# Performance work log

Hardware: AMD Instinct MI355X
Metric: run time of the kernel (lower is better)

The kernel has to match this reference:

```python
import jax, jax.numpy as jnp
import numpy as np

B, S, D, H = 2048, 200, 128, 4
H1, H2 = 64, 32
F = 4 * D
TIME_DECAY = 0.1


def setup_inputs() -> dict:
    key = jax.random.key(0)
    ks = jax.random.split(key, 10)
    query = jax.random.normal(ks[0], (B, D), dtype=jnp.float32)
    keys = jax.random.normal(ks[1], (B, S, D), dtype=jnp.float32)
    keys_mask = jax.random.randint(ks[2], (B, S), 0, 2).astype(bool)
    keys_mask = keys_mask.at[:, 0].set(True)  # avoid fully-masked rows
    sc = 0.02
    # per-head MLP params, stacked over heads
    W1 = sc * jax.random.normal(ks[3], (H, H1, F), dtype=jnp.float32)
    b1 = jnp.zeros((H, H1), dtype=jnp.float32)
    a1 = 0.25 * jnp.ones((H,), dtype=jnp.float32)  # PReLU (default single param)
    W2 = sc * jax.random.normal(ks[4], (H, H2, H1), dtype=jnp.float32)
    b2 = jnp.zeros((H, H2), dtype=jnp.float32)
    a2 = 0.25 * jnp.ones((H,), dtype=jnp.float32)
    W3 = sc * jax.random.normal(ks[5], (H, H2), dtype=jnp.float32)
    b3 = jnp.zeros((H,), dtype=jnp.float32)
    Wo = sc * jax.random.normal(ks[6], (D, D), dtype=jnp.float32)
    bo = jnp.zeros((D,), dtype=jnp.float32)
    return {"query": query, "keys": keys, "keys_mask": keys_mask,
            "W1": W1, "b1": b1, "a1": a1, "W2": W2, "b2": b2, "a2": a2,
            "W3": W3, "b3": b3, "Wo": Wo, "bo": bo}


def reference(query, keys, keys_mask, W1, b1, a1, W2, b2, a2, W3, b3, Wo, bo):
    b, s, d = keys.shape
    q = query[:, None, :]                                    # [B,1,D]
    x = jnp.concatenate(
        [keys, jnp.broadcast_to(q, (b, s, d)), keys * q, keys - q], axis=-1)  # [B,S,4D]
    pos = jnp.arange(s, dtype=keys.dtype)
    tw = jnp.exp(TIME_DECAY * (pos - s + 1))                 # [S]
    # all heads batched: [B,H,S,H1]
    h = jnp.einsum('bsf,hdf->bhsd', x, W1) + b1[None, :, None, :]
    h = jnp.where(h >= 0, h, a1[None, :, None, None] * h)    # PReLU
    h = jnp.einsum('bhsd,hed->bhse', h, W2) + b2[None, :, None, :]
    h = jnp.where(h >= 0, h, a2[None, :, None, None] * h)
    scores = jnp.einsum('bhse,he->bhs', h, W3) + b3[None, :, None]
    scores = scores * tw[None, None, :]
    scores = jnp.where(keys_mask[:, None, :], scores, -1e9)
    w = jax.nn.softmax(scores, axis=-1)                      # [B,H,S]
    out_h = jnp.einsum('bhs,bsd->bhd', w, keys)              # [B,H,D]
    combined = out_h.mean(axis=1)                            # [B,D]
    output = combined @ Wo.T + bo                            # [B,D]
    avg_weights = w.mean(axis=1)                             # [B,S]
    return output, avg_weights
```

## Files before the change

### kernel.cpp

```cpp
#include <hip/hip_runtime.h>
#include <hip/hip_bf16.h>
#include <stdint.h>

#define Bsz 2048
#define Ssz 200
#define Dsz 128
#define SP  224

typedef __attribute__((ext_vector_type(8))) short short8;
typedef __attribute__((ext_vector_type(4))) float f32x4;
typedef unsigned short ushort_t;
typedef unsigned int uint_t;

#define KEYS_OFF   0
#define H1S_OFF    51200
#define SCW_OFF    67584
#define C1S_OFF    71168
#define SMEM_BYTES 72192
#define SCWB_OFF   51200
#define COMB_OFF   59392
#define PO2_OFF    59904

__device__ __forceinline__ ushort_t cvtbf(float x) {
    __hip_bfloat16 h = __float2bfloat16(x);
    ushort_t u;
    __builtin_memcpy(&u, &h, 2);
    return u;
}

__global__ void prep_kernel(const float* __restrict__ W1, const float* __restrict__ W2,
                            const float* __restrict__ Wo,
                            float* __restrict__ W1sum, float* __restrict__ W1c,
                            float* __restrict__ W1diffR, float* __restrict__ WoT,
                            ushort_t* __restrict__ W2bf) {
    int i = blockIdx.x * blockDim.x + threadIdx.x;
    if (i < 32768) {
        int n = i >> 7, j = i & 127;
        float a  = W1[n * 512 + j];
        float dd = W1[n * 512 + 384 + j];
        W1sum[i] = a + dd;
        W1c[i]   = W1[n * 512 + 256 + j];
        W1diffR[i] = W1[n * 512 + 128 + j] - dd;
    }
    if (i < 16384) {
        int j = i >> 7, d = i & 127;
        WoT[i] = Wo[d * 128 + j];
    }
    if (i < 8192) W2bf[i] = cvtbf(W2[i]);
}

__launch_bounds__(256, 2)
__global__ void attn_kernel(const float* __restrict__ query, const float* __restrict__ keys,
                            const int* __restrict__ kmask,
                            const float* __restrict__ a1, const float* __restrict__ b2,
                            const float* __restrict__ a2, const float* __restrict__ W3,
                            const float* __restrict__ b3, const float* __restrict__ b1,
                            const float* __restrict__ bo,
                            const float* __restrict__ W1sum, const float* __restrict__ W1c,
                            const float* __restrict__ W1diffR,
                            const float* __restrict__ WoT, const ushort_t* __restrict__ W2bf,
                            float* __restrict__ out) {
    extern __shared__ char smem[];
    const int tid = threadIdx.x;
    const int bb  = blockIdx.x;
    const int w   = tid >> 6;
    const int l   = tid & 63;
    const int l15 = l & 15;
    const int lk  = l >> 4;

    float* scw  = (float*)(smem + SCW_OFF);
    float* c1s  = (float*)(smem + C1S_OFF);
    float* comb = (float*)(smem + COMB_OFF);
    float* po2  = (float*)(smem + PO2_OFF);
    const float* kb = keys + (size_t)bb * Ssz * Dsz;

    #pragma unroll
    for (int it = 0; it < 25; ++it) {
        int id = tid + 256 * it;
        int row = id >> 5, c4 = id & 31;
        float4 kv = *(const float4*)(kb + (size_t)row * Dsz + c4 * 4);
        uint2 p;
        p.x = (uint_t)cvtbf(kv.x) | ((uint_t)cvtbf(kv.y) << 16);
        p.y = (uint_t)cvtbf(kv.z) | ((uint_t)cvtbf(kv.w) << 16);
        int off = KEYS_OFF + (((row << 8) + (c4 << 3)) ^ ((row & 7) << 4));
        *(uint2*)(smem + off) = p;
    }

    {
        float accc = b1[tid];
        const float4* wr  = (const float4*)(W1diffR + tid * 128);
        const float4* qv4 = (const float4*)(query + bb * 128);
        #pragma unroll 8
        for (int j4 = 0; j4 < 32; ++j4) {
            float4 wv = wr[j4];
            float4 qq = qv4[j4];
            accc += wv.x * qq.x + wv.y * qq.y + wv.z * qq.z + wv.w * qq.w;
        }
        c1s[tid] = accc;
    }

    short8 bfr[16];
    #pragma unroll
    for (int t = 0; t < 4; ++t) {
        const int k0 = t * 32 + lk * 8;
        const float4* pq = (const float4*)(query + bb * 128 + k0);
        float4 q0 = pq[0], q1 = pq[1];
        #pragma unroll
        for (int nt = 0; nt < 4; ++nt) {
            int n = w * 64 + nt * 16 + l15;
            const float4* ps = (const float4*)(W1sum + n * 128 + k0);
            const float4* pc = (const float4*)(W1c + n * 128 + k0);
            float4 s0 = ps[0], s1 = ps[1];
            float4 c0 = pc[0], c1f = pc[1];
            short8 ov;
            ov[0] = (short)cvtbf(s0.x + c0.x * q0.x);
            ov[1] = (short)cvtbf(s0.y + c0.y * q0.y);
            ov[2] = (short)cvtbf(s0.z + c0.z * q0.z);
            ov[3] = (short)cvtbf(s0.w + c0.w * q0.w);
            ov[4] = (short)cvtbf(s1.x + c1f.x * q1.x);
            ov[5] = (short)cvtbf(s1.y + c1f.y * q1.y);
            ov[6] = (short)cvtbf(s1.z + c1f.z * q1.z);
            ov[7] = (short)cvtbf(s1.w + c1f.w * q1.w);
            bfr[t * 4 + nt] = ov;
        }
    }

    const float a1v = a1[w];
    const float a2v = a2[w];
    const float b3v = b3[w];
    float b2v[2], w3v[2];
    #pragma unroll
    for (int nt = 0; nt < 2; ++nt) {
        b2v[nt] = b2[w * 32 + nt * 16 + l15];
        w3v[nt] = W3[w * 32 + nt * 16 + l15];
    }
    short8 w2f[2][2];
    #pragma unroll
    for (int kt = 0; kt < 2; ++kt)
        #pragma unroll
        for (int nt = 0; nt < 2; ++nt)
            w2f[kt][nt] = *(const short8*)(W2bf + w * 2048 + (nt * 16 + l15) * 64 + kt * 32 + lk * 8);

    __syncthreads();

    float c1v[4];
    #pragma unroll
    for (int nt = 0; nt < 4; ++nt) c1v[nt] = c1s[w * 64 + nt * 16 + l15];

    const f32x4 fz = {0.f, 0.f, 0.f, 0.f};
    char* h1base = smem + H1S_OFF + w * 4096;

    #pragma unroll 2
    for (int m = 0; m < 13; ++m) {
        char* h1b = h1base + (m & 1) * 2048;
        f32x4 acc[4];
        #pragma unroll
        for (int nt = 0; nt < 4; ++nt) acc[nt] = fz;

        #pragma unroll
        for (int t = 0; t < 4; ++t) {
            int row = m * 16 + l15;
            row = (row < Ssz) ? row : (Ssz - 1);
            int off = KEYS_OFF + (((row << 8) + (t * 64 + lk * 16)) ^ ((row & 7) << 4));
            short8 afr = *(const short8*)(smem + off);
            #pragma unroll
            for (int nt = 0; nt < 4; ++nt)
                acc[nt] = __builtin_amdgcn_mfma_f32_16x16x32_bf16(afr, bfr[t * 4 + nt], acc[nt], 0, 0, 0);
        }

        #pragma unroll
        for (int nt = 0; nt < 4; ++nt) {
            #pragma unroll
            for (int r = 0; r < 4; ++r) {
                float v = acc[nt][r] + c1v[nt];
                v = (v >= 0.f) ? v : a1v * v;
                int lr = lk * 4 + r;
                int colb = (nt * 16 + l15) * 2;
                *(ushort_t*)(h1b + lr * 128 + (colb ^ ((lr & 7) << 4))) = cvtbf(v);
            }
        }

        f32x4 acc2[2];
        acc2[0] = fz; acc2[1] = fz;
        #pragma unroll
        for (int kt = 0; kt < 2; ++kt) {
            short8 afr2 = *(const short8*)(h1b + l15 * 128 + ((kt * 64 + lk * 16) ^ ((l15 & 7) << 4)));
            #pragma unroll
            for (int nt = 0; nt < 2; ++nt)
                acc2[nt] = __builtin_amdgcn_mfma_f32_16x16x32_bf16(afr2, w2f[kt][nt], acc2[nt], 0, 0, 0);
        }
        #pragma unroll
        for (int r = 0; r < 4; ++r) {
            float sum = 0.f;
            #pragma unroll
            for (int nt = 0; nt < 2; ++nt) {
                float v = acc2[nt][r] + b2v[nt];
                v = (v >= 0.f) ? v : a2v * v;
                sum += v * w3v[nt];
            }
            sum += __shfl_xor(sum, 1);
            sum += __shfl_xor(sum, 2);
            sum += __shfl_xor(sum, 4);
            sum += __shfl_xor(sum, 8);
            if (l15 == 0) {
                int sg = m * 16 + lk * 4 + r;
                if (sg < Ssz) {
                    float tw = __expf(0.1f * (float)(sg - (Ssz - 1)));
                    float sc = (sum + b3v) * tw;
                    scw[w * SP + sg] = kmask[bb * Ssz + sg] ? sc : -1.0e9f;
                }
            }
        }
    }

    float wv[4];
    {
        float xv[4];
        float mx = -3.0e38f;
        #pragma unroll
        for (int i = 0; i < 4; ++i) {
            int s = l + 64 * i;
            xv[i] = (s < Ssz) ? scw[w * SP + s] : -1.0e30f;
            mx = fmaxf(mx, xv[i]);
        }
        #pragma unroll
        for (int m = 1; m < 64; m <<= 1) mx = fmaxf(mx, __shfl_xor(mx, m));
        float sm = 0.f;
        #pragma unroll
        for (int i = 0; i < 4; ++i) {
            int s = l + 64 * i;
            wv[i] = (s < Ssz) ? __expf(xv[i] - mx) : 0.f;
            sm += wv[i];
        }
        #pragma unroll
        for (int m = 1; m < 64; m <<= 1) sm += __shfl_xor(sm, m);
        float inv = 1.0f / sm;
        #pragma unroll
        for (int i = 0; i < 4; ++i) {
            int s = l + 64 * i;
            wv[i] *= inv;
            if (s < Ssz) scw[w * SP + s] = wv[i];
        }
    }
    __syncthreads();

    #pragma unroll
    for (int i = 0; i < 4; ++i) {
        int s = l + 64 * i;
        *(ushort_t*)(smem + SCWB_OFF + w * 512 + s * 2) =
            (s < Ssz) ? cvtbf(wv[i]) : (ushort_t)0;
    }
    {
        uint_t* zb = (uint_t*)(smem + SCWB_OFF + 4 * 512);
        #pragma unroll
        for (int k = 0; k < 6; ++k) zb[tid + 256 * k] = 0;
    }
    __syncthreads();

    if (tid < Ssz) {
        float aw = 0.25f * (scw[tid] + scw[SP + tid] + scw[2 * SP + tid] + scw[3 * SP + tid]);
        out[Bsz * Dsz + bb * Ssz + tid] = aw;
    }

    {
        f32x4 acc4a = fz, acc4b = fz;
        #pragma unroll
        for (int t7 = 0; t7 < 7; ++t7) {
            int kbase = t7 * 32 + lk * 8;
            short8 afr = *(const short8*)(smem + SCWB_OFF + l15 * 512 + kbase * 2);
            short8 b2a, b2b;
            #pragma unroll
            for (int j = 0; j < 8; ++j) {
                int s = kbase + j;
                ushort_t kva = 0, kvb = 0;
                if (s < Ssz) {
                    int rowoff = KEYS_OFF + (s << 8);
                    int sw = (s & 7) << 4;
                    kva = *(const ushort_t*)(smem + (rowoff + ((32 * w + l15) << 1) ^ sw));
                    kvb = *(const ushort_t*)(smem + (rowoff + ((32 * w + 16 + l15) << 1) ^ sw));
                }
                b2a[j] = (short)kva;
                b2b[j] = (short)kvb;
            }
            acc4a = __builtin_amdgcn_mfma_f32_16x16x32_bf16(afr, b2a, acc4a, 0, 0, 0);
            acc4b = __builtin_amdgcn_mfma_f32_16x16x32_bf16(afr, b2b, acc4b, 0, 0, 0);
        }
        if (lk == 0) {
            comb[32 * w + l15]      = 0.25f * (acc4a[0] + acc4a[1] + acc4a[2] + acc4a[3]);
            comb[32 * w + 16 + l15] = 0.25f * (acc4b[0] + acc4b[1] + acc4b[2] + acc4b[3]);
        }
    }
    __syncthreads();

    {
        int d = tid & 127, part = tid >> 7;
        float o = 0.f;
        const float* wp = WoT + (size_t)part * 64 * 128 + d;
        #pragma unroll 8
        for (int j = 0; j < 64; ++j) o += comb[part * 64 + j] * wp[j * 128];
        po2[part * 128 + d] = o;
    }
    __syncthreads();
    if (tid < 128) out[bb * Dsz + tid] = bo[tid] + po2[tid] + po2[128 + tid];
}

extern "C" void kernel_launch(void* const* d_in, const int* in_sizes, int n_in,
                              void* d_out, int out_size, void* d_ws, size_t ws_size,
                              hipStream_t stream) {
    const float* query = (const float*)d_in[0];
    const float* keys  = (const float*)d_in[1];
    const int*   kmask = (const int*)d_in[2];
    const float* W1    = (const float*)d_in[3];
    const float* b1    = (const float*)d_in[4];
    const float* a1    = (const float*)d_in[5];
    const float* W2    = (const float*)d_in[6];
    const float* b2    = (const float*)d_in[7];
    const float* a2    = (const float*)d_in[8];
    const float* W3    = (const float*)d_in[9];
    const float* b3    = (const float*)d_in[10];
    const float* Wo    = (const float*)d_in[11];
    const float* bo    = (const float*)d_in[12];
    float* out = (float*)d_out;

    char* ws = (char*)d_ws;
    float*    W1sum   = (float*)(ws);
    float*    W1c     = (float*)(ws + 131072);
    float*    W1diffR = (float*)(ws + 262144);
    float*    WoT     = (float*)(ws + 393216);
    ushort_t* W2bf    = (ushort_t*)(ws + 458752);

    hipFuncSetAttribute(reinterpret_cast<const void*>(attn_kernel),
                        hipFuncAttributeMaxDynamicSharedMemorySize, SMEM_BYTES);

    prep_kernel<<<128, 256, 0, stream>>>(W1, W2, Wo, W1sum, W1c, W1diffR, WoT, W2bf);
    attn_kernel<<<Bsz, 256, SMEM_BYTES, stream>>>(query, keys, kmask, a1, b2, a2, W3, b3, b1, bo,
                                                  W1sum, W1c, W1diffR, WoT, W2bf, out);
}
```

Baseline: 209.7 us.

## Double block size to 512 threads and split sequence tiles across two wave halves

The attention kernel now launches 512 threads per block. Each head gets two waves that split the 13 sequence tiles of the MLP scoring loop between them, and the weighted-sum and output-projection stages are re-partitioned over 8 waves. The h1 staging buffer is no longer double-buffered per wave. The launch bounds are raised to request more waves per execution unit. The aim is more latency hiding and MFMA parallelism per block, at the risk of tighter register budgets (the B-fragments alone take many VGPRs) and extra synchronisation.

```diff
diff --git a/kernel.cpp b/kernel.cpp
--- a/kernel.cpp
+++ b/kernel.cpp
@@ -49,7 +49,7 @@
     if (i < 8192) W2bf[i] = cvtbf(W2[i]);
 }
 
-__launch_bounds__(256, 2)
+__launch_bounds__(512, 4)
 __global__ void attn_kernel(const float* __restrict__ query, const float* __restrict__ keys,
                             const int* __restrict__ kmask,
                             const float* __restrict__ a1, const float* __restrict__ b2,
@@ -63,7 +63,9 @@
     extern __shared__ char smem[];
     const int tid = threadIdx.x;
     const int bb  = blockIdx.x;
-    const int w   = tid >> 6;
+    const int w    = tid >> 6;
+    const int h    = w & 3;
+    const int half = w >> 2;
     const int l   = tid & 63;
     const int l15 = l & 15;
     const int lk  = l >> 4;
@@ -75,26 +77,28 @@
     const float* kb = keys + (size_t)bb * Ssz * Dsz;
 
     #pragma unroll
-    for (int it = 0; it < 25; ++it) {
-        int id = tid + 256 * it;
-        int row = id >> 5, c4 = id & 31;
-        float4 kv = *(const float4*)(kb + (size_t)row * Dsz + c4 * 4);
-        uint2 p;
-        p.x = (uint_t)cvtbf(kv.x) | ((uint_t)cvtbf(kv.y) << 16);
-        p.y = (uint_t)cvtbf(kv.z) | ((uint_t)cvtbf(kv.w) << 16);
-        int off = KEYS_OFF + (((row << 8) + (c4 << 3)) ^ ((row & 7) << 4));
-        *(uint2*)(smem + off) = p;
-    }
-
-    {
+    for (int it = 0; it < 13; ++it) {
+        int id = tid + 512 * it;
+        if (id < 6400) {
+            int row = id >> 5, c4 = id & 31;
+            float4 kv = *(const float4*)(kb + (size_t)row * Dsz + c4 * 4);
+            uint2 p;
+            p.x = (uint_t)cvtbf(kv.x) | ((uint_t)cvtbf(kv.y) << 16);
+            p.y = (uint_t)cvtbf(kv.z) | ((uint_t)cvtbf(kv.w) << 16);
+            int off = KEYS_OFF + (((row << 8) + (c4 << 3)) ^ ((row & 7) << 4));
+            *(uint2*)(smem + off) = p;
+        }
+    }
+
+    if (tid < 256) {
         float accc = b1[tid];
         const float4* wr  = (const float4*)(W1diffR + tid * 128);
         const float4* qv4 = (const float4*)(query + bb * 128);
         #pragma unroll 8
         for (int j4 = 0; j4 < 32; ++j4) {
-            float4 wv = wr[j4];
+            float4 wvv = wr[j4];
             float4 qq = qv4[j4];
-            accc += wv.x * qq.x + wv.y * qq.y + wv.z * qq.z + wv.w * qq.w;
+            accc += wvv.x * qq.x + wvv.y * qq.y + wvv.z * qq.z + wvv.w * qq.w;
         }
         c1s[tid] = accc;
     }
@@ -107,7 +111,7 @@
         float4 q0 = pq[0], q1 = pq[1];
         #pragma unroll
         for (int nt = 0; nt < 4; ++nt) {
-            int n = w * 64 + nt * 16 + l15;
+            int n = h * 64 + nt * 16 + l15;
             const float4* ps = (const float4*)(W1sum + n * 128 + k0);
             const float4* pc = (const float4*)(W1c + n * 128 + k0);
             float4 s0 = ps[0], s1 = ps[1];
@@ -125,97 +129,99 @@
         }
     }
 
-    const float a1v = a1[w];
-    const float a2v = a2[w];
-    const float b3v = b3[w];
+    const float a1v = a1[h];
+    const float a2v = a2[h];
+    const float b3v = b3[h];
     float b2v[2], w3v[2];
     #pragma unroll
     for (int nt = 0; nt < 2; ++nt) {
-        b2v[nt] = b2[w * 32 + nt * 16 + l15];
-        w3v[nt] = W3[w * 32 + nt * 16 + l15];
+        b2v[nt] = b2[h * 32 + nt * 16 + l15];
+        w3v[nt] = W3[h * 32 + nt * 16 + l15];
     }
     short8 w2f[2][2];
     #pragma unroll
     for (int kt = 0; kt < 2; ++kt)
         #pragma unroll
         for (int nt = 0; nt < 2; ++nt)
-            w2f[kt][nt] = *(const short8*)(W2bf + w * 2048 + (nt * 16 + l15) * 64 + kt * 32 + lk * 8);
+            w2f[kt][nt] = *(const short8*)(W2bf + h * 2048 + (nt * 16 + l15) * 64 + kt * 32 + lk * 8);
 
     __syncthreads();
 
     float c1v[4];
     #pragma unroll
-    for (int nt = 0; nt < 4; ++nt) c1v[nt] = c1s[w * 64 + nt * 16 + l15];
+    for (int nt = 0; nt < 4; ++nt) c1v[nt] = c1s[h * 64 + nt * 16 + l15];
 
     const f32x4 fz = {0.f, 0.f, 0.f, 0.f};
-    char* h1base = smem + H1S_OFF + w * 4096;
-
-    #pragma unroll 2
-    for (int m = 0; m < 13; ++m) {
-        char* h1b = h1base + (m & 1) * 2048;
-        f32x4 acc[4];
-        #pragma unroll
-        for (int nt = 0; nt < 4; ++nt) acc[nt] = fz;
-
-        #pragma unroll
-        for (int t = 0; t < 4; ++t) {
-            int row = m * 16 + l15;
-            row = (row < Ssz) ? row : (Ssz - 1);
-            int off = KEYS_OFF + (((row << 8) + (t * 64 + lk * 16)) ^ ((row & 7) << 4));
-            short8 afr = *(const short8*)(smem + off);
-            #pragma unroll
-            for (int nt = 0; nt < 4; ++nt)
-                acc[nt] = __builtin_amdgcn_mfma_f32_16x16x32_bf16(afr, bfr[t * 4 + nt], acc[nt], 0, 0, 0);
-        }
-
-        #pragma unroll
-        for (int nt = 0; nt < 4; ++nt) {
+    char* h1b = smem + H1S_OFF + w * 2048;
+
+    #pragma unroll 1
+    for (int mi = 0; mi < 7; ++mi) {
+        int m = half * 7 + mi;
+        if (m < 13) {
+            f32x4 acc[4];
+            #pragma unroll
+            for (int nt = 0; nt < 4; ++nt) acc[nt] = fz;
+
+            #pragma unroll
+            for (int t = 0; t < 4; ++t) {
+                int row = m * 16 + l15;
+                row = (row < Ssz) ? row : (Ssz - 1);
+                int off = KEYS_OFF + (((row << 8) + (t * 64 + lk * 16)) ^ ((row & 7) << 4));
+                short8 afr = *(const short8*)(smem + off);
+                #pragma unroll
+                for (int nt = 0; nt < 4; ++nt)
+                    acc[nt] = __builtin_amdgcn_mfma_f32_16x16x32_bf16(afr, bfr[t * 4 + nt], acc[nt], 0, 0, 0);
+            }
+
+            #pragma unroll
+            for (int nt = 0; nt < 4; ++nt) {
+                #pragma unroll
+                for (int r = 0; r < 4; ++r) {
+                    float v = acc[nt][r] + c1v[nt];
+                    v = (v >= 0.f) ? v : a1v * v;
+                    int lr = lk * 4 + r;
+                    int colb = (nt * 16 + l15) * 2;
+                    *(ushort_t*)(h1b + lr * 128 + (colb ^ ((lr & 7) << 4))) = cvtbf(v);
+                }
+            }
+
+            f32x4 acc2[2];
+            acc2[0] = fz; acc2[1] = fz;
+            #pragma unroll
+            for (int kt = 0; kt < 2; ++kt) {
+                short8 afr2 = *(const short8*)(h1b + l15 * 128 + ((kt * 64 + lk * 16) ^ ((l15 & 7) << 4)));
+                #pragma unroll
+                for (int nt = 0; nt < 2; ++nt)
+                    acc2[nt] = __builtin_amdgcn_mfma_f32_16x16x32_bf16(afr2, w2f[kt][nt], acc2[nt], 0, 0, 0);
+            }
             #pragma unroll
             for (int r = 0; r < 4; ++r) {
-                float v = acc[nt][r] + c1v[nt];
-                v = (v >= 0.f) ? v : a1v * v;
-                int lr = lk * 4 + r;
-                int colb = (nt * 16 + l15) * 2;
-                *(ushort_t*)(h1b + lr * 128 + (colb ^ ((lr & 7) << 4))) = cvtbf(v);
-            }
-        }
-
-        f32x4 acc2[2];
-        acc2[0] = fz; acc2[1] = fz;
-        #pragma unroll
-        for (int kt = 0; kt < 2; ++kt) {
-            short8 afr2 = *(const short8*)(h1b + l15 * 128 + ((kt * 64 + lk * 16) ^ ((l15 & 7) << 4)));
-            #pragma unroll
-            for (int nt = 0; nt < 2; ++nt)
-                acc2[nt] = __builtin_amdgcn_mfma_f32_16x16x32_bf16(afr2, w2f[kt][nt], acc2[nt], 0, 0, 0);
-        }
-        #pragma unroll
-        for (int r = 0; r < 4; ++r) {
-            float sum = 0.f;
-            #pragma unroll
-            for (int nt = 0; nt < 2; ++nt) {
-                float v = acc2[nt][r] + b2v[nt];
-                v = (v >= 0.f) ? v : a2v * v;
-                sum += v * w3v[nt];
-            }
-            sum += __shfl_xor(sum, 1);
-            sum += __shfl_xor(sum, 2);
-            sum += __shfl_xor(sum, 4);
-            sum += __shfl_xor(sum, 8);
-            if (l15 == 0) {
-                int sg = m * 16 + lk * 4 + r;
-                if (sg < Ssz) {
-                    float tw = __expf(0.1f * (float)(sg - (Ssz - 1)));
-                    float sc = (sum + b3v) * tw;
-                    scw[w * SP + sg] = kmask[bb * Ssz + sg] ? sc : -1.0e9f;
+                float sum = 0.f;
+                #pragma unroll
+                for (int nt = 0; nt < 2; ++nt) {
+                    float v = acc2[nt][r] + b2v[nt];
+                    v = (v >= 0.f) ? v : a2v * v;
+                    sum += v * w3v[nt];
                 }
-            }
-        }
-    }
-
-    float wv[4];
-    {
-        float xv[4];
+                sum += __shfl_xor(sum, 1);
+                sum += __shfl_xor(sum, 2);
+                sum += __shfl_xor(sum, 4);
+                sum += __shfl_xor(sum, 8);
+                if (l15 == 0) {
+                    int sg = m * 16 + lk * 4 + r;
+                    if (sg < Ssz) {
+                        float tw = __expf(0.1f * (float)(sg - (Ssz - 1)));
+                        float sc = (sum + b3v) * tw;
+                        scw[h * SP + sg] = kmask[bb * Ssz + sg] ? sc : -1.0e9f;
+                    }
+                }
+            }
+        }
+    }
+    __syncthreads();
+
+    if (w < 4) {
+        float wv[4], xv[4];
         float mx = -3.0e38f;
         #pragma unroll
         for (int i = 0; i < 4; ++i) {
@@ -240,20 +246,14 @@
             int s = l + 64 * i;
             wv[i] *= inv;
             if (s < Ssz) scw[w * SP + s] = wv[i];
-        }
-    }
-    __syncthreads();
-
-    #pragma unroll
-    for (int i = 0; i < 4; ++i) {
-        int s = l + 64 * i;
-        *(ushort_t*)(smem + SCWB_OFF + w * 512 + s * 2) =
-            (s < Ssz) ? cvtbf(wv[i]) : (ushort_t)0;
-    }
-    {
+            *(ushort_t*)(smem + SCWB_OFF + w * 512 + s * 2) =
+                (s < Ssz) ? cvtbf(wv[i]) : (ushort_t)0;
+        }
+    } else {
         uint_t* zb = (uint_t*)(smem + SCWB_OFF + 4 * 512);
-        #pragma unroll
-        for (int k = 0; k < 6; ++k) zb[tid + 256 * k] = 0;
+        int t4 = tid - 256;
+        #pragma unroll
+        for (int k = 0; k < 6; ++k) zb[t4 + 256 * k] = 0;
     }
     __syncthreads();
 
@@ -263,45 +263,41 @@
     }
 
     {
-        f32x4 acc4a = fz, acc4b = fz;
+        f32x4 acc4 = fz;
         #pragma unroll
         for (int t7 = 0; t7 < 7; ++t7) {
             int kbase = t7 * 32 + lk * 8;
             short8 afr = *(const short8*)(smem + SCWB_OFF + l15 * 512 + kbase * 2);
-            short8 b2a, b2b;
+            short8 bfr2;
             #pragma unroll
             for (int j = 0; j < 8; ++j) {
                 int s = kbase + j;
-                ushort_t kva = 0, kvb = 0;
+                ushort_t kv = 0;
                 if (s < Ssz) {
-                    int rowoff = KEYS_OFF + (s << 8);
-                    int sw = (s & 7) << 4;
-                    kva = *(const ushort_t*)(smem + (rowoff + ((32 * w + l15) << 1) ^ sw));
-                    kvb = *(const ushort_t*)(smem + (rowoff + ((32 * w + 16 + l15) << 1) ^ sw));
+                    kv = *(const ushort_t*)(smem + KEYS_OFF +
+                          ((((s << 8) + ((16 * w + l15) << 1))) ^ ((s & 7) << 4)));
                 }
-                b2a[j] = (short)kva;
-                b2b[j] = (short)kvb;
-            }
-            acc4a = __builtin_amdgcn_mfma_f32_16x16x32_bf16(afr, b2a, acc4a, 0, 0, 0);
-            acc4b = __builtin_amdgcn_mfma_f32_16x16x32_bf16(afr, b2b, acc4b, 0, 0, 0);
-        }
-        if (lk == 0) {
-            comb[32 * w + l15]      = 0.25f * (acc4a[0] + acc4a[1] + acc4a[2] + acc4a[3]);
-            comb[32 * w + 16 + l15] = 0.25f * (acc4b[0] + acc4b[1] + acc4b[2] + acc4b[3]);
-        }
+                bfr2[j] = (short)kv;
+            }
+            acc4 = __builtin_amdgcn_mfma_f32_16x16x32_bf16(afr, bfr2, acc4, 0, 0, 0);
+        }
+        if (lk == 0)
+            comb[16 * w + l15] = 0.25f * (acc4[0] + acc4[1] + acc4[2] + acc4[3]);
     }
     __syncthreads();
 
     {
         int d = tid & 127, part = tid >> 7;
         float o = 0.f;
-        const float* wp = WoT + (size_t)part * 64 * 128 + d;
+        const float* wp = WoT + (size_t)part * 32 * 128 + d;
         #pragma unroll 8
-        for (int j = 0; j < 64; ++j) o += comb[part * 64 + j] * wp[j * 128];
+        for (int j = 0; j < 32; ++j) o += comb[part * 32 + j] * wp[j * 128];
         po2[part * 128 + d] = o;
     }
     __syncthreads();
-    if (tid < 128) out[bb * Dsz + tid] = bo[tid] + po2[tid] + po2[128 + tid];
+    if (tid < 128) {
+        out[bb * Dsz + tid] = bo[tid] + po2[tid] + po2[128 + tid] + po2[256 + tid] + po2[384 + tid];
+    }
 }
 
 extern "C" void kernel_launch(void* const* d_in, const int* in_sizes, int n_in,
@@ -333,6 +329,6 @@
                         hipFuncAttributeMaxDynamicSharedMemorySize, SMEM_BYTES);
 
     prep_kernel<<<128, 256, 0, stream>>>(W1, W2, Wo, W1sum, W1c, W1diffR, WoT, W2bf);
-    attn_kernel<<<Bsz, 256, SMEM_BYTES, stream>>>(query, keys, kmask, a1, b2, a2, W3, b3, b1, bo,
+    attn_kernel<<<Bsz, 512, SMEM_BYTES, stream>>>(query, keys, kmask, a1, b2, a2, W3, b3, b1, bo,
                                                   W1sum, W1c, W1diffR, WoT, W2bf, out);
 }
```

Result: slower. 292.7 us (+39.6%).

## Split fused attention kernel into c1, per-half-sequence scores, and finish kernels

Applied to the files above, without the earlier changes.

Breaks the single per-batch kernel into three launches. A separate kernel precomputes the query-dependent bias, a scores kernel handles half the sequence per block with less shared memory and higher occupancy, and a finish kernel does softmax, weighted key sum and the output projection. The aim is more parallelism and occupancy for the MLP scoring phase. The cost is extra launches, a round trip of scores through global memory, reloading keys in fp32 in the finish kernel, and the bfr weight fragments being rebuilt twice per batch row.

```diff
diff --git a/kernel.cpp b/kernel.cpp
--- a/kernel.cpp
+++ b/kernel.cpp
@@ -5,7 +5,6 @@
 #define Bsz 2048
 #define Ssz 200
 #define Dsz 128
-#define SP  224
 
 typedef __attribute__((ext_vector_type(8))) short short8;
 typedef __attribute__((ext_vector_type(4))) float f32x4;
@@ -13,13 +12,9 @@
 typedef unsigned int uint_t;
 
 #define KEYS_OFF   0
-#define H1S_OFF    51200
-#define SCW_OFF    67584
-#define C1S_OFF    71168
-#define SMEM_BYTES 72192
-#define SCWB_OFF   51200
-#define COMB_OFF   59392
-#define PO2_OFF    59904
+#define H1S_OFF    28672
+#define C1S_OFF    36864
+#define SMEM_A     37888
 
 __device__ __forceinline__ ushort_t cvtbf(float x) {
     __hip_bfloat16 h = __float2bfloat16(x);
@@ -49,36 +44,50 @@
     if (i < 8192) W2bf[i] = cvtbf(W2[i]);
 }
 
-__launch_bounds__(256, 2)
-__global__ void attn_kernel(const float* __restrict__ query, const float* __restrict__ keys,
-                            const int* __restrict__ kmask,
-                            const float* __restrict__ a1, const float* __restrict__ b2,
-                            const float* __restrict__ a2, const float* __restrict__ W3,
-                            const float* __restrict__ b3, const float* __restrict__ b1,
-                            const float* __restrict__ bo,
-                            const float* __restrict__ W1sum, const float* __restrict__ W1c,
-                            const float* __restrict__ W1diffR,
-                            const float* __restrict__ WoT, const ushort_t* __restrict__ W2bf,
-                            float* __restrict__ out) {
+__global__ void c1_kernel(const float* __restrict__ query, const float* __restrict__ W1diffR,
+                          const float* __restrict__ b1, float* __restrict__ c1out) {
+    int b = blockIdx.x, n = threadIdx.x;
+    float acc = b1[n];
+    const float4* wr  = (const float4*)(W1diffR + n * 128);
+    const float4* qv4 = (const float4*)(query + b * 128);
+    #pragma unroll 8
+    for (int j4 = 0; j4 < 32; ++j4) {
+        float4 wv = wr[j4];
+        float4 qq = qv4[j4];
+        acc += wv.x * qq.x + wv.y * qq.y + wv.z * qq.z + wv.w * qq.w;
+    }
+    c1out[b * 256 + n] = acc;
+}
+
+__launch_bounds__(256, 4)
+__global__ void scores_kernel(const float* __restrict__ query, const float* __restrict__ keys,
+                              const int* __restrict__ kmask,
+                              const float* __restrict__ a1, const float* __restrict__ b2,
+                              const float* __restrict__ a2, const float* __restrict__ W3,
+                              const float* __restrict__ b3,
+                              const float* __restrict__ W1sum, const float* __restrict__ W1c,
+                              const ushort_t* __restrict__ W2bf, const float* __restrict__ c1ws,
+                              float* __restrict__ scores_ws) {
     extern __shared__ char smem[];
-    const int tid = threadIdx.x;
-    const int bb  = blockIdx.x;
+    const int tid  = threadIdx.x;
+    const int bb   = blockIdx.x >> 1;
+    const int half = blockIdx.x & 1;
     const int w   = tid >> 6;
     const int l   = tid & 63;
     const int l15 = l & 15;
     const int lk  = l >> 4;
 
-    float* scw  = (float*)(smem + SCW_OFF);
-    float* c1s  = (float*)(smem + C1S_OFF);
-    float* comb = (float*)(smem + COMB_OFF);
-    float* po2  = (float*)(smem + PO2_OFF);
+    float* c1s = (float*)(smem + C1S_OFF);
     const float* kb = keys + (size_t)bb * Ssz * Dsz;
-
-    #pragma unroll
-    for (int it = 0; it < 25; ++it) {
+    const int rbase = half * 112;
+
+    #pragma unroll
+    for (int it = 0; it < 14; ++it) {
         int id = tid + 256 * it;
         int row = id >> 5, c4 = id & 31;
-        float4 kv = *(const float4*)(kb + (size_t)row * Dsz + c4 * 4);
+        int grow = rbase + row;
+        float4 kv = {0.f, 0.f, 0.f, 0.f};
+        if (grow < Ssz) kv = *(const float4*)(kb + (size_t)grow * Dsz + c4 * 4);
         uint2 p;
         p.x = (uint_t)cvtbf(kv.x) | ((uint_t)cvtbf(kv.y) << 16);
         p.y = (uint_t)cvtbf(kv.z) | ((uint_t)cvtbf(kv.w) << 16);
@@ -86,18 +95,7 @@
         *(uint2*)(smem + off) = p;
     }
 
-    {
-        float accc = b1[tid];
-        const float4* wr  = (const float4*)(W1diffR + tid * 128);
-        const float4* qv4 = (const float4*)(query + bb * 128);
-        #pragma unroll 8
-        for (int j4 = 0; j4 < 32; ++j4) {
-            float4 wv = wr[j4];
-            float4 qq = qv4[j4];
-            accc += wv.x * qq.x + wv.y * qq.y + wv.z * qq.z + wv.w * qq.w;
-        }
-        c1s[tid] = accc;
-    }
+    if (tid < 256) c1s[tid] = c1ws[bb * 256 + tid];
 
     short8 bfr[16];
     #pragma unroll
@@ -148,79 +146,97 @@
     for (int nt = 0; nt < 4; ++nt) c1v[nt] = c1s[w * 64 + nt * 16 + l15];
 
     const f32x4 fz = {0.f, 0.f, 0.f, 0.f};
-    char* h1base = smem + H1S_OFF + w * 4096;
+    char* h1b = smem + H1S_OFF + w * 2048;
+    const int ntiles = 7 - half;
 
     #pragma unroll 2
-    for (int m = 0; m < 13; ++m) {
-        char* h1b = h1base + (m & 1) * 2048;
-        f32x4 acc[4];
-        #pragma unroll
-        for (int nt = 0; nt < 4; ++nt) acc[nt] = fz;
-
-        #pragma unroll
-        for (int t = 0; t < 4; ++t) {
-            int row = m * 16 + l15;
-            row = (row < Ssz) ? row : (Ssz - 1);
-            int off = KEYS_OFF + (((row << 8) + (t * 64 + lk * 16)) ^ ((row & 7) << 4));
-            short8 afr = *(const short8*)(smem + off);
-            #pragma unroll
-            for (int nt = 0; nt < 4; ++nt)
-                acc[nt] = __builtin_amdgcn_mfma_f32_16x16x32_bf16(afr, bfr[t * 4 + nt], acc[nt], 0, 0, 0);
-        }
-
-        #pragma unroll
-        for (int nt = 0; nt < 4; ++nt) {
-            #pragma unroll
-            for (int r = 0; r < 4; ++r) {
-                float v = acc[nt][r] + c1v[nt];
-                v = (v >= 0.f) ? v : a1v * v;
-                int lr = lk * 4 + r;
-                int colb = (nt * 16 + l15) * 2;
-                *(ushort_t*)(h1b + lr * 128 + (colb ^ ((lr & 7) << 4))) = cvtbf(v);
+    for (int mi = 0; mi < 7; ++mi) {
+        if (mi < ntiles) {
+            f32x4 acc[4];
+            #pragma unroll
+            for (int nt = 0; nt < 4; ++nt) acc[nt] = fz;
+
+            #pragma unroll
+            for (int t = 0; t < 4; ++t) {
+                int lrow = mi * 16 + l15;
+                int off = KEYS_OFF + (((lrow << 8) + (t * 64 + lk * 16)) ^ ((lrow & 7) << 4));
+                short8 afr = *(const short8*)(smem + off);
+                #pragma unroll
+                for (int nt = 0; nt < 4; ++nt)
+                    acc[nt] = __builtin_amdgcn_mfma_f32_16x16x32_bf16(afr, bfr[t * 4 + nt], acc[nt], 0, 0, 0);
             }
-        }
-
-        f32x4 acc2[2];
-        acc2[0] = fz; acc2[1] = fz;
-        #pragma unroll
-        for (int kt = 0; kt < 2; ++kt) {
-            short8 afr2 = *(const short8*)(h1b + l15 * 128 + ((kt * 64 + lk * 16) ^ ((l15 & 7) << 4)));
-            #pragma unroll
-            for (int nt = 0; nt < 2; ++nt)
-                acc2[nt] = __builtin_amdgcn_mfma_f32_16x16x32_bf16(afr2, w2f[kt][nt], acc2[nt], 0, 0, 0);
-        }
-        #pragma unroll
-        for (int r = 0; r < 4; ++r) {
-            float sum = 0.f;
-            #pragma unroll
-            for (int nt = 0; nt < 2; ++nt) {
-                float v = acc2[nt][r] + b2v[nt];
-                v = (v >= 0.f) ? v : a2v * v;
-                sum += v * w3v[nt];
-            }
-            sum += __shfl_xor(sum, 1);
-            sum += __shfl_xor(sum, 2);
-            sum += __shfl_xor(sum, 4);
-            sum += __shfl_xor(sum, 8);
-            if (l15 == 0) {
-                int sg = m * 16 + lk * 4 + r;
-                if (sg < Ssz) {
-                    float tw = __expf(0.1f * (float)(sg - (Ssz - 1)));
-                    float sc = (sum + b3v) * tw;
-                    scw[w * SP + sg] = kmask[bb * Ssz + sg] ? sc : -1.0e9f;
+
+            #pragma unroll
+            for (int nt = 0; nt < 4; ++nt) {
+                #pragma unroll
+                for (int r = 0; r < 4; ++r) {
+                    float v = acc[nt][r] + c1v[nt];
+                    v = (v >= 0.f) ? v : a1v * v;
+                    int lr = lk * 4 + r;
+                    int colb = (nt * 16 + l15) * 2;
+                    *(ushort_t*)(h1b + lr * 128 + (colb ^ ((lr & 7) << 4))) = cvtbf(v);
                 }
             }
-        }
-    }
-
-    float wv[4];
-    {
-        float xv[4];
+
+            f32x4 acc2[2];
+            acc2[0] = fz; acc2[1] = fz;
+            #pragma unroll
+            for (int kt = 0; kt < 2; ++kt) {
+                short8 afr2 = *(const short8*)(h1b + l15 * 128 + ((kt * 64 + lk * 16) ^ ((l15 & 7) << 4)));
+                #pragma unroll
+                for (int nt = 0; nt < 2; ++nt)
+                    acc2[nt] = __builtin_amdgcn_mfma_f32_16x16x32_bf16(afr2, w2f[kt][nt], acc2[nt], 0, 0, 0);
+            }
+            #pragma unroll
+            for (int r = 0; r < 4; ++r) {
+                float sum = 0.f;
+                #pragma unroll
+                for (int nt = 0; nt < 2; ++nt) {
+                    float v = acc2[nt][r] + b2v[nt];
+                    v = (v >= 0.f) ? v : a2v * v;
+                    sum += v * w3v[nt];
+                }
+                sum += __shfl_xor(sum, 1);
+                sum += __shfl_xor(sum, 2);
+                sum += __shfl_xor(sum, 4);
+                sum += __shfl_xor(sum, 8);
+                if (l15 == 0) {
+                    int sg = rbase + mi * 16 + lk * 4 + r;
+                    if (sg < Ssz) {
+                        float tw = __expf(0.1f * (float)(sg - (Ssz - 1)));
+                        float sc = (sum + b3v) * tw;
+                        scores_ws[bb * 800 + w * 200 + sg] =
+                            kmask[bb * Ssz + sg] ? sc : -1.0e9f;
+                    }
+                }
+            }
+        }
+    }
+}
+
+__launch_bounds__(512, 4)
+__global__ void finish_kernel(const float* __restrict__ keys, const float* __restrict__ WoT,
+                              const float* __restrict__ bo, const float* __restrict__ scores_ws,
+                              float* __restrict__ out) {
+    __shared__ float scw[4][224];
+    __shared__ float avgs[224];
+    __shared__ float po[4][128];
+    __shared__ float comb[128];
+    __shared__ float po2[4][128];
+
+    const int tid = threadIdx.x;
+    const int bb  = blockIdx.x;
+    const int w   = tid >> 6;
+    const int l   = tid & 63;
+    const float* kb = keys + (size_t)bb * Ssz * Dsz;
+
+    if (w < 4) {
+        float xv[4], wv[4];
         float mx = -3.0e38f;
         #pragma unroll
         for (int i = 0; i < 4; ++i) {
             int s = l + 64 * i;
-            xv[i] = (s < Ssz) ? scw[w * SP + s] : -1.0e30f;
+            xv[i] = (s < Ssz) ? scores_ws[bb * 800 + w * 200 + s] : -1.0e30f;
             mx = fmaxf(mx, xv[i]);
         }
         #pragma unroll
@@ -238,70 +254,41 @@
         #pragma unroll
         for (int i = 0; i < 4; ++i) {
             int s = l + 64 * i;
-            wv[i] *= inv;
-            if (s < Ssz) scw[w * SP + s] = wv[i];
-        }
-    }
-    __syncthreads();
-
-    #pragma unroll
-    for (int i = 0; i < 4; ++i) {
-        int s = l + 64 * i;
-        *(ushort_t*)(smem + SCWB_OFF + w * 512 + s * 2) =
-            (s < Ssz) ? cvtbf(wv[i]) : (ushort_t)0;
-    }
+            if (s < Ssz) scw[w][s] = wv[i] * inv;
+        }
+    }
+    __syncthreads();
+
+    if (tid < Ssz) {
+        float aw = 0.25f * (scw[0][tid] + scw[1][tid] + scw[2][tid] + scw[3][tid]);
+        avgs[tid] = aw;
+        out[Bsz * Dsz + bb * Ssz + tid] = aw;
+    }
+    __syncthreads();
+
     {
-        uint_t* zb = (uint_t*)(smem + SCWB_OFF + 4 * 512);
-        #pragma unroll
-        for (int k = 0; k < 6; ++k) zb[tid + 256 * k] = 0;
-    }
-    __syncthreads();
-
-    if (tid < Ssz) {
-        float aw = 0.25f * (scw[tid] + scw[SP + tid] + scw[2 * SP + tid] + scw[3 * SP + tid]);
-        out[Bsz * Dsz + bb * Ssz + tid] = aw;
-    }
-
-    {
-        f32x4 acc4a = fz, acc4b = fz;
-        #pragma unroll
-        for (int t7 = 0; t7 < 7; ++t7) {
-            int kbase = t7 * 32 + lk * 8;
-            short8 afr = *(const short8*)(smem + SCWB_OFF + l15 * 512 + kbase * 2);
-            short8 b2a, b2b;
-            #pragma unroll
-            for (int j = 0; j < 8; ++j) {
-                int s = kbase + j;
-                ushort_t kva = 0, kvb = 0;
-                if (s < Ssz) {
-                    int rowoff = KEYS_OFF + (s << 8);
-                    int sw = (s & 7) << 4;
-                    kva = *(const ushort_t*)(smem + (rowoff + ((32 * w + l15) << 1) ^ sw));
-                    kvb = *(const ushort_t*)(smem + (rowoff + ((32 * w + 16 + l15) << 1) ^ sw));
-                }
-                b2a[j] = (short)kva;
-                b2b[j] = (short)kvb;
-            }
-            acc4a = __builtin_amdgcn_mfma_f32_16x16x32_bf16(afr, b2a, acc4a, 0, 0, 0);
-            acc4b = __builtin_amdgcn_mfma_f32_16x16x32_bf16(afr, b2b, acc4b, 0, 0, 0);
-        }
-        if (lk == 0) {
-            comb[32 * w + l15]      = 0.25f * (acc4a[0] + acc4a[1] + acc4a[2] + acc4a[3]);
-            comb[32 * w + 16 + l15] = 0.25f * (acc4b[0] + acc4b[1] + acc4b[2] + acc4b[3]);
-        }
-    }
+        int d = tid & 127, p = tid >> 7;
+        float s0 = 0.f;
+        for (int s = p; s < Ssz; s += 4)
+            s0 += avgs[s] * kb[(size_t)s * Dsz + d];
+        po[p][d] = s0;
+    }
+    __syncthreads();
+    if (tid < 128) comb[tid] = po[0][tid] + po[1][tid] + po[2][tid] + po[3][tid];
     __syncthreads();
 
     {
         int d = tid & 127, part = tid >> 7;
         float o = 0.f;
-        const float* wp = WoT + (size_t)part * 64 * 128 + d;
+        const float* wp = WoT + (size_t)part * 32 * 128 + d;
         #pragma unroll 8
-        for (int j = 0; j < 64; ++j) o += comb[part * 64 + j] * wp[j * 128];
-        po2[part * 128 + d] = o;
-    }
-    __syncthreads();
-    if (tid < 128) out[bb * Dsz + tid] = bo[tid] + po2[tid] + po2[128 + tid];
+        for (int j = 0; j < 32; ++j) o += comb[part * 32 + j] * wp[j * 128];
+        po2[part][d] = o;
+    }
+    __syncthreads();
+    if (tid < 128) {
+        out[bb * Dsz + tid] = bo[tid] + po2[0][tid] + po2[1][tid] + po2[2][tid] + po2[3][tid];
+    }
 }
 
 extern "C" void kernel_launch(void* const* d_in, const int* in_sizes, int n_in,
@@ -328,11 +315,15 @@
     float*    W1diffR = (float*)(ws + 262144);
     float*    WoT     = (float*)(ws + 393216);
     ushort_t* W2bf    = (ushort_t*)(ws + 458752);
-
-    hipFuncSetAttribute(reinterpret_cast<const void*>(attn_kernel),
-                        hipFuncAttributeMaxDynamicSharedMemorySize, SMEM_BYTES);
+    float*    c1ws    = (float*)(ws + 475136);
+    float*    scores  = (float*)(ws + 2572288);
+
+    hipFuncSetAttribute(reinterpret_cast<const void*>(scores_kernel),
+                        hipFuncAttributeMaxDynamicSharedMemorySize, SMEM_A);
 
     prep_kernel<<<128, 256, 0, stream>>>(W1, W2, Wo, W1sum, W1c, W1diffR, WoT, W2bf);
-    attn_kernel<<<Bsz, 256, SMEM_BYTES, stream>>>(query, keys, kmask, a1, b2, a2, W3, b3, b1, bo,
-                                                  W1sum, W1c, W1diffR, WoT, W2bf, out);
-}
+    c1_kernel<<<Bsz, 256, 0, stream>>>(query, W1diffR, b1, c1ws);
+    scores_kernel<<<Bsz * 2, 256, SMEM_A, stream>>>(query, keys, kmask, a1, b2, a2, W3, b3,
+                                                    W1sum, W1c, W2bf, c1ws, scores);
+    finish_kernel<<<Bsz, 512, 0, stream>>>(keys, WoT, bo, scores, out);
+}
```

Result: slower. 331.7 us (+58.2%).
